# Performance work log

Hardware: AMD Instinct MI355X
Metric: run time of the kernel (lower is better)

The kernel has to match this reference:

```python
import jax, jax.numpy as jnp
import numpy as np

NUM_HEADS = 8
DIM = 256
HEAD_DIM = DIM // NUM_HEADS  # 32
CPB_HIDDEN = 512
FFN_HIDDEN = 1024


def _relative_position_cpb(query_size, key_size, pretrain_size):
    # TransNeXt-style continuous position bias table + index (query==key grid here)
    qh, qw = query_size
    kh, kw = key_size
    ph, pw = pretrain_size
    aqh = np.arange(qh, dtype=np.float64)
    akh = np.arange(kh, dtype=np.float64)
    aqw = np.arange(qw, dtype=np.float64)
    akw = np.arange(kw, dtype=np.float64)
    kH, kW = np.meshgrid(akh, akw, indexing='ij')
    qH, qW = np.meshgrid(aqh, aqw, indexing='ij')
    rel_h = (qH.reshape(-1)[:, None] - kH.reshape(-1)[None, :]) / (ph - 1) * 8.0
    rel_w = (qW.reshape(-1)[:, None] - kW.reshape(-1)[None, :]) / (pw - 1) * 8.0
    rel = np.stack([rel_h, rel_w], axis=-1).reshape(-1, 2)
    table, idx = np.unique(rel, return_inverse=True, axis=0)
    table = np.sign(table) * np.log2(np.abs(table) + 1.0) / np.log2(8.0)
    return idx.astype(np.int32).reshape(-1), table.astype(np.float32)


def setup_inputs() -> dict:
    key = jax.random.key(0)
    ks = jax.random.split(key, 16)
    B, C, H, W = 8, 256, 128, 128
    q = jax.random.normal(ks[0], (B, C, H, W), dtype=jnp.float32)
    kv = jax.random.normal(ks[1], (B, C, H, W), dtype=jnp.float32)
    rel_idx_np, rel_table_np = _relative_position_cpb((32, 32), (32, 32), (32, 32))
    s = 0.02
    inp = {
        'q': q,
        'kv': kv,
        'rel_pos_index': jnp.asarray(rel_idx_np),
        'rel_coords_table': jnp.asarray(rel_table_np),
        'Wq': jax.random.normal(ks[2], (DIM, DIM), jnp.float32) * s,
        'bq': jnp.zeros((DIM,), jnp.float32),
        'Wkv': jax.random.normal(ks[3], (DIM, 2 * DIM), jnp.float32) * s,
        'bkv': jnp.zeros((2 * DIM,), jnp.float32),
        'Wo': jax.random.normal(ks[4], (DIM, DIM), jnp.float32) * s,
        'bo': jnp.zeros((DIM,), jnp.float32),
        'cpb_w1': jax.random.normal(ks[5], (2, CPB_HIDDEN), jnp.float32) * s,
        'cpb_b1': jnp.zeros((CPB_HIDDEN,), jnp.float32),
        'cpb_w2': jax.random.normal(ks[6], (CPB_HIDDEN, NUM_HEADS), jnp.float32) * s,
        'cpb_b2': jnp.zeros((NUM_HEADS,), jnp.float32),
        'ffn_w1': jax.random.normal(ks[7], (DIM, FFN_HIDDEN), jnp.float32) * s,
        'ffn_b1': jnp.zeros((FFN_HIDDEN,), jnp.float32),
        'ffn_w2': jax.random.normal(ks[8], (FFN_HIDDEN, DIM), jnp.float32) * s,
        'ffn_b2': jnp.zeros((DIM,), jnp.float32),
        'ln_g': jnp.ones((DIM,), jnp.float32),
        'ln_b': jnp.zeros((DIM,), jnp.float32),
    }
    return inp


def _resize_bilinear(x, size):
    # matches torch F.interpolate(mode='bilinear', align_corners=False)
    return jax.image.resize(x, (x.shape[0], x.shape[1], size[0], size[1]),
                            method='linear', antialias=False)


def _layernorm(x, g, b, eps=1e-5):
    mu = jnp.mean(x, axis=-1, keepdims=True)
    var = jnp.mean(jnp.square(x - mu), axis=-1, keepdims=True)
    return (x - mu) * jax.lax.rsqrt(var + eps) * g + b


def _fpn_forward(q, kv, rel_pos_index, rel_coords_table, Wq, bq, Wkv, bkv, Wo, bo,
                 cpb_w1, cpb_b1, cpb_w2, cpb_b2, ffn_w1, ffn_b1, ffn_w2, ffn_b2, ln_g, ln_b):
    x = q
    B, C, H, W = q.shape
    pH = H // 4
    pW = H // 4  # note: original code uses h for both, matching square inputs
    N = pH * pW

    qd = jax.nn.relu(_resize_bilinear(q, (pH, pW)))   # [B,C,pH,pW] (dropout p=0)
    kvd = jax.nn.relu(_resize_bilinear(kv, (pH, pW)))
    qt = qd.reshape(B, C, N).transpose(0, 2, 1)   # [B,N,C]
    kvt = kvd.reshape(B, C, N).transpose(0, 2, 1)  # [B,N,C]

    # --- BVAM: cross-attention with continuous relative position bias ---
    qh = (qt @ Wq + bq).reshape(B, N, NUM_HEADS, HEAD_DIM).transpose(0, 2, 1, 3)  # [B,h,N,d]
    kvp = (kvt @ Wkv + bkv).reshape(B, N, 2, NUM_HEADS, HEAD_DIM).transpose(2, 0, 3, 1, 4)
    k, v = kvp[0], kvp[1]  # [B,h,N,d]

    cpb = jax.nn.relu(rel_coords_table @ cpb_w1 + cpb_b1) @ cpb_w2 + cpb_b2  # [L,h]
    bias = cpb[rel_pos_index].reshape(N, N, NUM_HEADS).transpose(2, 0, 1)    # [h,N,N]

    scale = 1.0 / jnp.sqrt(jnp.float32(HEAD_DIM))
    logits = jnp.einsum('bhnd,bhmd->bhnm', qh, k) * scale + bias[None]
    attn = jax.nn.softmax(logits, axis=-1)
    out = jnp.einsum('bhnm,bhmd->bhnd', attn, v)
    out = out.transpose(0, 2, 1, 3).reshape(B, N, C) @ Wo + bo  # [B,N,C]

    # --- FFN (post-norm, gelu) ---
    ff = jax.nn.gelu(out @ ffn_w1 + ffn_b1, approximate=False) @ ffn_w2 + ffn_b2
    y = _layernorm(out + ff, ln_g, ln_b)  # [B,N,C]

    # back to spatial, upsample, residual
    y = y.transpose(0, 2, 1).reshape(B, C, pH, pW)
    y = jax.nn.relu(_resize_bilinear(y, (H, W)))
    return x + y


def reference(q, kv, rel_pos_index, rel_coords_table, Wq, bq, Wkv, bkv, Wo, bo,
              cpb_w1, cpb_b1, cpb_w2, cpb_b2, ffn_w1, ffn_b1, ffn_w2, ffn_b2, ln_g, ln_b):
    return _fpn_forward(q, kv, rel_pos_index, rel_coords_table, Wq, bq, Wkv, bkv, Wo, bo,
                        cpb_w1, cpb_b1, cpb_w2, cpb_b2, ffn_w1, ffn_b1, ffn_w2, ffn_b2, ln_g, ln_b)
```

## Files before the change

kernel.cpp:

```cpp
#include <hip/hip_runtime.h>
#include <hip/hip_bf16.h>
#include <hip/hip_fp16.h>

typedef __hip_bfloat16 bf16;
typedef __attribute__((ext_vector_type(8))) __bf16 bf16x8;
typedef __attribute__((ext_vector_type(4))) __bf16 bf16x4;
typedef __attribute__((ext_vector_type(4))) float f32x4;
typedef __attribute__((ext_vector_type(4))) float f4;

__device__ __forceinline__ void gload_lds16(const bf16* g, bf16* l)
{
    __builtin_amdgcn_global_load_lds((const __attribute__((address_space(1))) void*)g,
                                     (__attribute__((address_space(3))) void*)l, 16, 0, 0);
}

__global__ __launch_bounds__(256) void prep_kernel(
    const float* __restrict__ tab, const float* __restrict__ w1, const float* __restrict__ b1,
    const float* __restrict__ w2, const float* __restrict__ b2, float* __restrict__ cpbout, int L, int ncpb,
    const float* __restrict__ Wq, const float* __restrict__ Wkv, const float* __restrict__ Wo,
    const float* __restrict__ fw1, const float* __restrict__ fw2,
    bf16* __restrict__ WqT, bf16* __restrict__ WkvT, bf16* __restrict__ WoT,
    bf16* __restrict__ W1T, bf16* __restrict__ W2T,
    const float* __restrict__ qsrc, const float* __restrict__ kvsrc,
    bf16* __restrict__ qdst, bf16* __restrict__ kvdst)
{
    __shared__ float o[32][33];
    const int t = threadIdx.x;
    int bid = blockIdx.x;
    if (bid < ncpb) {
        int l = bid * 32 + (t >> 3);
        int js = t & 7;
        bool valid = l < L;
        float t0 = valid ? tab[2 * l] : 0.f, t1 = valid ? tab[2 * l + 1] : 0.f;
        float acc[8];
#pragma unroll
        for (int hh = 0; hh < 8; ++hh) acc[hh] = 0.f;
        for (int j = js; j < 512; j += 8) {
            float hv = fmaxf(t0 * w1[j] + t1 * w1[512 + j] + b1[j], 0.f);
            f4 w2a = *(const f4*)&w2[j * 8];
            f4 w2b = *(const f4*)&w2[j * 8 + 4];
#pragma unroll
            for (int hh = 0; hh < 4; ++hh) { acc[hh] += hv * w2a[hh]; acc[4 + hh] += hv * w2b[hh]; }
        }
#pragma unroll
        for (int d = 1; d < 8; d <<= 1)
#pragma unroll
            for (int hh = 0; hh < 8; ++hh) acc[hh] += __shfl_xor(acc[hh], d);
        if (js == 0 && valid)
#pragma unroll
            for (int hh = 0; hh < 8; ++hh) cpbout[(size_t)hh * L + l] = acc[hh] + b2[hh];
        return;
    }
    bid -= ncpb;
    if (bid < 3072) {
        const float* W; bf16* WT; int K, N, base;
        if (bid < 256)       { W = Wq;  WT = WqT;  K = 256;  N = 256;  base = 0; }
        else if (bid < 768)  { W = Wkv; WT = WkvT; K = 256;  N = 512;  base = 256; }
        else if (bid < 1024) { W = Wo;  WT = WoT;  K = 256;  N = 256;  base = 768; }
        else if (bid < 2048) { W = fw1; WT = W1T;  K = 256;  N = 1024; base = 1024; }
        else                 { W = fw2; WT = W2T;  K = 1024; N = 256;  base = 2048; }
        int idx = (bid - base) * 256 + t;
        int n = idx / K, k = idx % K;
        WT[idx] = (bf16)W[(size_t)k * N + n];
        return;
    }
    bid -= 3072;
    {
        const float* src = bid < 2048 ? qsrc : kvsrc;
        bf16* dst = bid < 2048 ? qdst : kvdst;
        int bb2 = bid & 2047;
        int cc = bb2 & 7, i = (bb2 >> 3) & 31, b = bb2 >> 8;
#pragma unroll
        for (int p = 0; p < 4; ++p) {
            int id = p * 256 + t;
            int c = id >> 5, j = id & 31;
            const float* r = src + ((size_t)(b * 256 + cc * 32 + c) * 128 + 4 * i + 1) * 128 + 4 * j;
            float4 r1 = *(const float4*)r;
            float4 r2 = *(const float4*)(r + 128);
            o[c][j] = 0.25f * (r1.y + r1.z + r2.y + r2.z);
        }
        __syncthreads();
#pragma unroll
        for (int p = 0; p < 4; ++p) {
            int id = p * 256 + t;
            int j = id >> 5, c = id & 31;
            dst[(size_t)(b * 1024 + i * 32 + j) * 256 + cc * 32 + c] = (bf16)fmaxf(o[c][j], 0.f);
        }
    }
}

__global__ __launch_bounds__(256) void bias_gather_kernel(
    const int* __restrict__ ridx, const float* __restrict__ cpbh,
    bf16* __restrict__ biasF, int L)
{
    int gid = blockIdx.x * 256 + threadIdx.x;
    int ls = gid & 63;
    int mt = (gid >> 6) & 31;
    int qt = gid >> 11;
    int lo = ls & 15, hi = ls >> 4;
    int idx[2][8];
#pragma unroll
    for (int qj = 0; qj < 2; ++qj)
#pragma unroll
        for (int j = 0; j < 8; ++j) {
            int kf = j >> 2, r = j & 3;
            int q = qt * 32 + qj * 16 + lo;
            int m = mt * 32 + kf * 16 + hi * 4 + r;
            idx[qj][j] = ridx[q * 1024 + m];
        }
    for (int h = 0; h < 8; ++h) {
        const float* ct = cpbh + (size_t)h * L;
#pragma unroll
        for (int qj = 0; qj < 2; ++qj) {
            bf16 vals[8];
#pragma unroll
            for (int j = 0; j < 8; ++j) vals[j] = (bf16)ct[idx[qj][j]];
            size_t off = ((((size_t)(h * 32 + qt) * 32 + mt) * 2 + qj) * 64 + ls) * 8;
            *(bf16x8*)&biasF[off] = *(const bf16x8*)vals;
        }
    }
}

template<int BM, int BN>
__global__ __launch_bounds__(256) void gemm_bt(
    const bf16* __restrict__ A, const bf16* __restrict__ BT,
    const float* __restrict__ bias, bf16* __restrict__ Cb, float* __restrict__ Cf,
    const bf16* __restrict__ resid, int M, int N, int K, int act)
{
    constexpr int MI = BM / 32;
    constexpr int NJ = BN / 32;
    __shared__ __align__(16) bf16 As[BM * 64];
    __shared__ __align__(16) bf16 Bs[BN * 64];
    const int tid = threadIdx.x;
    const int lane = tid & 63, wid = tid >> 6;
    const int lo = lane & 15, hi = lane >> 4;
    const int m0 = blockIdx.x * BM, n0 = blockIdx.y * BN;
    const int wr = wid >> 1, wc = wid & 1;
    f32x4 acc[MI][NJ];
#pragma unroll
    for (int i = 0; i < MI; ++i)
#pragma unroll
        for (int j = 0; j < NJ; ++j) acc[i][j] = f32x4{0.f, 0.f, 0.f, 0.f};

    for (int k0 = 0; k0 < K; k0 += 64) {
        __syncthreads();
#pragma unroll
        for (int p = 0; p < BM / 32; ++p) {
            int f = p * 256 + wid * 64 + lane;
            int row = f >> 3, cs = f & 7;
            gload_lds16(&A[(size_t)(m0 + row) * K + k0 + ((cs ^ (row & 7)) * 8)],
                        As + (size_t)(p * 256 + wid * 64) * 8);
        }
#pragma unroll
        for (int p = 0; p < BN / 32; ++p) {
            int f = p * 256 + wid * 64 + lane;
            int row = f >> 3, cs = f & 7;
            gload_lds16(&BT[(size_t)(n0 + row) * K + k0 + ((cs ^ (row & 7)) * 8)],
                        Bs + (size_t)(p * 256 + wid * 64) * 8);
        }
        __syncthreads();
        bf16x8 af[2][MI], bfr[2][NJ];
#pragma unroll
        for (int kk = 0; kk < 2; ++kk) {
#pragma unroll
            for (int i = 0; i < MI; ++i) {
                int row = wr * (BM / 2) + i * 16 + lo;
                af[kk][i] = *(const bf16x8*)&As[row * 64 + (((kk * 4 + hi) ^ (lo & 7)) * 8)];
            }
#pragma unroll
            for (int j = 0; j < NJ; ++j) {
                int row = wc * (BN / 2) + j * 16 + lo;
                bfr[kk][j] = *(const bf16x8*)&Bs[row * 64 + (((kk * 4 + hi) ^ (lo & 7)) * 8)];
            }
        }
#pragma unroll
        for (int kk = 0; kk < 2; ++kk)
#pragma unroll
            for (int i = 0; i < MI; ++i)
#pragma unroll
                for (int j = 0; j < NJ; ++j)
                    acc[i][j] = __builtin_amdgcn_mfma_f32_16x16x32_bf16(af[kk][i], bfr[kk][j], acc[i][j], 0, 0, 0);
    }
#pragma unroll
    for (int i = 0; i < MI; ++i)
#pragma unroll
        for (int j = 0; j < NJ; ++j) {
            int col = n0 + wc * (BN / 2) + j * 16 + lo;
            float bv = bias[col];
#pragma unroll
            for (int r = 0; r < 4; ++r) {
                int row = m0 + wr * (BM / 2) + i * 16 + hi * 4 + r;
                float v = acc[i][j][r] + bv;
                if (act == 1) v = 0.5f * v * (1.f + erff(v * 0.70710678118654752f));
                if (resid) v += (float)resid[(size_t)row * N + col];
                if (Cb) Cb[(size_t)row * N + col] = (bf16)v;
                else    Cf[(size_t)row * N + col] = v;
            }
        }
}

__global__ __launch_bounds__(256) void ffn2_ln_kernel(
    const bf16* __restrict__ A, const bf16* __restrict__ BT,
    const float* __restrict__ bias, const bf16* __restrict__ resid,
    const float* __restrict__ g, const float* __restrict__ bb,
    bf16* __restrict__ ysp)
{
    __shared__ __align__(16) bf16 As[32 * 64];
    __shared__ __align__(16) bf16 Bs[256 * 64];
    __shared__ float buf[32][260];
    const int tid = threadIdx.x;
    const int lane = tid & 63, wid = tid >> 6;
    const int lo = lane & 15, hi = lane >> 4;
    const int m0 = blockIdx.x * 32;
    f32x4 acc[2][4];
#pragma unroll
    for (int i = 0; i < 2; ++i)
#pragma unroll
        for (int j = 0; j < 4; ++j) acc[i][j] = f32x4{0.f, 0.f, 0.f, 0.f};

    for (int k0 = 0; k0 < 1024; k0 += 64) {
        __syncthreads();
        {
            int f = tid;
            int row = f >> 3, cs = f & 7;
            gload_lds16(&A[(size_t)(m0 + row) * 1024 + k0 + ((cs ^ (row & 7)) * 8)],
                        As + (size_t)(wid * 64) * 8);
        }
#pragma unroll
        for (int p = 0; p < 8; ++p) {
            int f = p * 256 + tid;
            int row = f >> 3, cs = f & 7;
            gload_lds16(&BT[(size_t)row * 1024 + k0 + ((cs ^ (row & 7)) * 8)],
                        Bs + (size_t)(p * 256 + wid * 64) * 8);
        }
        __syncthreads();
        bf16x8 af[2][2], bfr[2][4];
#pragma unroll
        for (int kk = 0; kk < 2; ++kk) {
#pragma unroll
            for (int i = 0; i < 2; ++i) {
                int row = i * 16 + lo;
                af[kk][i] = *(const bf16x8*)&As[row * 64 + (((kk * 4 + hi) ^ (lo & 7)) * 8)];
            }
#pragma unroll
            for (int j = 0; j < 4; ++j) {
                int row = wid * 64 + j * 16 + lo;
                bfr[kk][j] = *(const bf16x8*)&Bs[row * 64 + (((kk * 4 + hi) ^ (lo & 7)) * 8)];
            }
        }
#pragma unroll
        for (int kk = 0; kk < 2; ++kk)
#pragma unroll
            for (int i = 0; i < 2; ++i)
#pragma unroll
                for (int j = 0; j < 4; ++j)
                    acc[i][j] = __builtin_amdgcn_mfma_f32_16x16x32_bf16(af[kk][i], bfr[kk][j], acc[i][j], 0, 0, 0);
    }
#pragma unroll
    for (int i = 0; i < 2; ++i)
#pragma unroll
        for (int j = 0; j < 4; ++j) {
            int col = wid * 64 + j * 16 + lo;
            float bv = bias[col];
#pragma unroll
            for (int r = 0; r < 4; ++r) {
                int lr = i * 16 + hi * 4 + r;
                buf[lr][col] = acc[i][j][r] + bv + (float)resid[(size_t)(m0 + lr) * 256 + col];
            }
        }
    __syncthreads();
#pragma unroll
    for (int rr = 0; rr < 8; ++rr) {
        int row = wid * 8 + rr;
        f4 x = *(const f4*)&buf[row][lane * 4];
        float s = x[0] + x[1] + x[2] + x[3];
#pragma unroll
        for (int d = 1; d < 64; d <<= 1) s += __shfl_xor(s, d);
        float mean = s * (1.f / 256.f);
        f4 dv = {x[0] - mean, x[1] - mean, x[2] - mean, x[3] - mean};
        float s2 = dv[0] * dv[0] + dv[1] * dv[1] + dv[2] * dv[2] + dv[3] * dv[3];
#pragma unroll
        for (int d = 1; d < 64; d <<= 1) s2 += __shfl_xor(s2, d);
        float rstd = rsqrtf(s2 * (1.f / 256.f) + 1e-5f);
        f4 o = {dv[0] * rstd, dv[1] * rstd, dv[2] * rstd, dv[3] * rstd};
        *(f4*)&buf[row][lane * 4] = o;
    }
    __syncthreads();
    float gc = g[tid], bc = bb[tid];
    int b = m0 >> 10, n0l = m0 & 1023;
    bf16* dst = &ysp[((size_t)(b * 256 + tid) << 10) + n0l];
#pragma unroll
    for (int p = 0; p < 4; ++p) {
        bf16 tmp[8];
#pragma unroll
        for (int k = 0; k < 8; ++k) tmp[k] = (bf16)(buf[p * 8 + k][tid] * gc + bc);
        *(bf16x8*)&dst[p * 8] = *(const bf16x8*)tmp;
    }
}

__global__ __launch_bounds__(256) void vtrans_kernel(const bf16* __restrict__ kvp,
                                                     bf16* __restrict__ vT)
{
    __shared__ __align__(16) bf16 tile[64][40];
    int bid = blockIdx.x;
    int mc = bid & 15, h = (bid >> 4) & 7, b = bid >> 7;
    int t = threadIdx.x;
    {
        int m = t >> 2, p = (t & 3) * 8;
        *(float4*)&tile[m][p] =
            *(const float4*)&kvp[(size_t)(b * 1024 + mc * 64 + m) * 512 + 256 + h * 32 + p];
    }
    __syncthreads();
#pragma unroll
    for (int it = 0; it < 8; ++it) {
        int f = it * 256 + t;
        int d = f >> 6, m = f & 63;
        vT[(size_t)((b * 8 + h) * 32 + d) * 1024 + mc * 64 + m] = tile[m][d];
    }
}

__global__ __launch_bounds__(256) void attn_kernel(
    const bf16* __restrict__ qh, const bf16* __restrict__ kvp, const bf16* __restrict__ vT,
    const bf16* __restrict__ biasF, bf16* __restrict__ attnout)
{
    __shared__ __align__(16) bf16 Ps[4][32 * 40];
    __shared__ __align__(16) __half accs[4][32][34];
    __shared__ float pm[4][32], pl[4][32];
    const int tid = threadIdx.x, lane = tid & 63, wid = tid >> 6;
    const int lo = lane & 15, hi = lane >> 4;
    const int qt = blockIdx.x, n0 = qt * 32;
    const int h = blockIdx.y;
    const int b = blockIdx.z;
    const float scale = 0.17677669529663687f;
    const f32x4 zero4 = {0.f, 0.f, 0.f, 0.f};

    bf16x8 qf[2];
#pragma unroll
    for (int qj = 0; qj < 2; ++qj)
        qf[qj] = *(const bf16x8*)&qh[(size_t)(b * 1024 + n0 + qj * 16 + lo) * 256 + h * 32 + hi * 8];

    f32x4 acc[2][2];
#pragma unroll
    for (int i = 0; i < 2; ++i)
#pragma unroll
        for (int j = 0; j < 2; ++j) acc[i][j] = zero4;
    float mrow[2] = {-1e30f, -1e30f}, lrow[2] = {0.f, 0.f};

    bf16* Pw = Ps[wid];

    for (int t = wid; t < 32; t += 4) {
        const int m0 = t * 32;
        bf16x8 kfr0 = *(const bf16x8*)&kvp[(size_t)(b * 1024 + m0 + lo) * 512 + h * 32 + hi * 8];
        bf16x8 kfr1 = *(const bf16x8*)&kvp[(size_t)(b * 1024 + m0 + 16 + lo) * 512 + h * 32 + hi * 8];
        bf16x8 va0 = *(const bf16x8*)&vT[(size_t)((b * 8 + h) * 32 + lo) * 1024 + m0 + hi * 8];
        bf16x8 va1 = *(const bf16x8*)&vT[(size_t)((b * 8 + h) * 32 + 16 + lo) * 1024 + m0 + hi * 8];
        size_t boff = (((size_t)(h * 32 + qt) * 32 + t) * 2 * 64 + lane) * 8;
        bf16x8 bv0 = *(const bf16x8*)&biasF[boff];
        bf16x8 bv1 = *(const bf16x8*)&biasF[boff + 512];

        f32x4 s[2][2];
        s[0][0] = __builtin_amdgcn_mfma_f32_16x16x32_bf16(kfr0, qf[0], zero4, 0, 0, 0);
        s[0][1] = __builtin_amdgcn_mfma_f32_16x16x32_bf16(kfr0, qf[1], zero4, 0, 0, 0);
        s[1][0] = __builtin_amdgcn_mfma_f32_16x16x32_bf16(kfr1, qf[0], zero4, 0, 0, 0);
        s[1][1] = __builtin_amdgcn_mfma_f32_16x16x32_bf16(kfr1, qf[1], zero4, 0, 0, 0);
#pragma unroll
        for (int kf = 0; kf < 2; ++kf)
#pragma unroll
            for (int r = 0; r < 4; ++r) {
                s[kf][0][r] = s[kf][0][r] * scale + (float)bv0[kf * 4 + r];
                s[kf][1][r] = s[kf][1][r] * scale + (float)bv1[kf * 4 + r];
            }
#pragma unroll
        for (int qj = 0; qj < 2; ++qj) {
            float mx = fmaxf(fmaxf(fmaxf(s[0][qj][0], s[0][qj][1]), fmaxf(s[0][qj][2], s[0][qj][3])),
                             fmaxf(fmaxf(s[1][qj][0], s[1][qj][1]), fmaxf(s[1][qj][2], s[1][qj][3])));
            mx = fmaxf(mx, __shfl_xor(mx, 16));
            mx = fmaxf(mx, __shfl_xor(mx, 32));
            float mnew = fmaxf(mrow[qj], mx);
            float alpha = __expf(mrow[qj] - mnew);
            float rs = 0.f;
#pragma unroll
            for (int kf = 0; kf < 2; ++kf)
#pragma unroll
                for (int r = 0; r < 4; ++r) {
                    float p = __expf(s[kf][qj][r] - mnew);
                    s[kf][qj][r] = p;
                    rs += p;
                }
            rs += __shfl_xor(rs, 16);
            rs += __shfl_xor(rs, 32);
            lrow[qj] = lrow[qj] * alpha + rs;
            mrow[qj] = mnew;
#pragma unroll
            for (int di = 0; di < 2; ++di)
#pragma unroll
                for (int r = 0; r < 4; ++r) acc[di][qj][r] *= alpha;
        }
#pragma unroll
        for (int qj = 0; qj < 2; ++qj)
#pragma unroll
            for (int kf = 0; kf < 2; ++kf)
#pragma unroll
                for (int r = 0; r < 4; ++r)
                    Pw[(qj * 16 + lo) * 40 + kf * 16 + hi * 4 + r] = (bf16)s[kf][qj][r];
        bf16x8 pb0 = *(const bf16x8*)&Pw[lo * 40 + hi * 8];
        bf16x8 pb1 = *(const bf16x8*)&Pw[(16 + lo) * 40 + hi * 8];
        acc[0][0] = __builtin_amdgcn_mfma_f32_16x16x32_bf16(va0, pb0, acc[0][0], 0, 0, 0);
        acc[0][1] = __builtin_amdgcn_mfma_f32_16x16x32_bf16(va0, pb1, acc[0][1], 0, 0, 0);
        acc[1][0] = __builtin_amdgcn_mfma_f32_16x16x32_bf16(va1, pb0, acc[1][0], 0, 0, 0);
        acc[1][1] = __builtin_amdgcn_mfma_f32_16x16x32_bf16(va1, pb1, acc[1][1], 0, 0, 0);
    }
#pragma unroll
    for (int di = 0; di < 2; ++di)
#pragma unroll
        for (int qj = 0; qj < 2; ++qj)
#pragma unroll
            for (int r = 0; r < 4; ++r)
                accs[wid][di * 16 + hi * 4 + r][qj * 16 + lo] = __float2half(acc[di][qj][r]);
    if (hi == 0) {
#pragma unroll
        for (int qj = 0; qj < 2; ++qj) {
            pm[wid][qj * 16 + lo] = mrow[qj];
            pl[wid][qj * 16 + lo] = lrow[qj];
        }
    }
    __syncthreads();
    int q = tid >> 3, d0 = (tid & 7) * 4;
    float M = fmaxf(fmaxf(pm[0][q], pm[1][q]), fmaxf(pm[2][q], pm[3][q]));
    float f0 = __expf(pm[0][q] - M), f1 = __expf(pm[1][q] - M);
    float f2 = __expf(pm[2][q] - M), f3 = __expf(pm[3][q] - M);
    float inv = 1.f / (pl[0][q] * f0 + pl[1][q] * f1 + pl[2][q] * f2 + pl[3][q] * f3);
    bf16 tmp[4];
#pragma unroll
    for (int j = 0; j < 4; ++j) {
        int d = d0 + j;
        float o = f0 * (float)accs[0][d][q] + f1 * (float)accs[1][d][q] +
                  f2 * (float)accs[2][d][q] + f3 * (float)accs[3][d][q];
        tmp[j] = (bf16)(o * inv);
    }
    *(bf16x4*)&attnout[(size_t)(b * 1024 + n0 + q) * 256 + h * 32 + d0] = *(const bf16x4*)tmp;
}

__global__ __launch_bounds__(256) void upsample_kernel(const float* __restrict__ x,
    const bf16* __restrict__ ysp, float* __restrict__ out)
{
    int idx = blockIdx.x * 256 + threadIdx.x;
    int w4 = idx & 31; int r1 = idx >> 5;
    int hh = r1 & 127; int r2 = r1 >> 7;
    int c = r2 & 255; int b = r2 >> 8;
    float chh = 0.25f * hh - 0.375f;
    float fi = floorf(chh);
    float fh = chh - fi;
    int i0 = (int)fi;
    int ia = i0 < 0 ? 0 : i0;
    int ib = (i0 + 1) > 31 ? 31 : (i0 + 1);
    const bf16* yr = ysp + ((size_t)(b * 256 + c) << 10);
    const bf16* ra = yr + ia * 32;
    const bf16* rb = yr + ib * 32;
    f4 xv = *(const f4*)&x[(size_t)idx * 4];
    f4 o;
#pragma unroll
    for (int k = 0; k < 4; ++k) {
        int ww = w4 * 4 + k;
        float cww = 0.25f * ww - 0.375f;
        float fj = floorf(cww);
        float fw = cww - fj;
        int j0 = (int)fj;
        int ja = j0 < 0 ? 0 : j0;
        int jb = (j0 + 1) > 31 ? 31 : (j0 + 1);
        float v = (1.f - fh) * ((1.f - fw) * (float)ra[ja] + fw * (float)ra[jb]) +
                  fh * ((1.f - fw) * (float)rb[ja] + fw * (float)rb[jb]);
        o[k] = xv[k] + fmaxf(v, 0.f);
    }
    *(f4*)&out[(size_t)idx * 4] = o;
}

extern "C" void kernel_launch(void* const* d_in, const int* in_sizes, int n_in,
                              void* d_out, int out_size, void* d_ws, size_t ws_size,
                              hipStream_t stream)
{
    (void)n_in; (void)out_size; (void)ws_size;
    const float* q    = (const float*)d_in[0];
    const float* kv   = (const float*)d_in[1];
    const int*   ridx = (const int*)d_in[2];
    const float* rtab = (const float*)d_in[3];
    const float* Wq   = (const float*)d_in[4];
    const float* bq   = (const float*)d_in[5];
    const float* Wkv  = (const float*)d_in[6];
    const float* bkv  = (const float*)d_in[7];
    const float* Wo   = (const float*)d_in[8];
    const float* bo   = (const float*)d_in[9];
    const float* cw1  = (const float*)d_in[10];
    const float* cb1  = (const float*)d_in[11];
    const float* cw2  = (const float*)d_in[12];
    const float* cb2  = (const float*)d_in[13];
    const float* fw1  = (const float*)d_in[14];
    const float* fb1  = (const float*)d_in[15];
    const float* fw2  = (const float*)d_in[16];
    const float* fb2  = (const float*)d_in[17];
    const float* lng  = (const float*)d_in[18];
    const float* lnb  = (const float*)d_in[19];
    const int L = in_sizes[3] / 2;
    const int ncpb = (L + 31) / 32;

    char* w = (char*)d_ws;
    auto alloc = [&](size_t bytes) { char* p = w; w += (bytes + 255) & ~(size_t)255; return p; };
    bf16* qt      = (bf16*)alloc(8192ull * 256 * 2);
    bf16* kvt     = (bf16*)alloc(8192ull * 256 * 2);
    bf16* qhb     = (bf16*)alloc(8192ull * 256 * 2);
    bf16* kvpb    = (bf16*)alloc(8192ull * 512 * 2);
    bf16* vTb     = (bf16*)alloc(8ull * 8 * 32 * 1024 * 2);
    bf16* attnb   = (bf16*)alloc(8192ull * 256 * 2);
    bf16* outb    = (bf16*)alloc(8192ull * 256 * 2);
    bf16* ffh     = (bf16*)alloc(8192ull * 1024 * 2);
    bf16* ysp     = (bf16*)alloc(8ull * 256 * 1024 * 2);
    bf16* WqT     = (bf16*)alloc(256ull * 256 * 2);
    bf16* WkvT    = (bf16*)alloc(512ull * 256 * 2);
    bf16* WoT     = (bf16*)alloc(256ull * 256 * 2);
    bf16* W1T     = (bf16*)alloc(1024ull * 256 * 2);
    bf16* W2T     = (bf16*)alloc(256ull * 1024 * 2);
    float* cpbb   = (float*)alloc((size_t)8 * L * 4);
    bf16* biasF   = ffh;

    prep_kernel<<<dim3(ncpb + 3072 + 4096), 256, 0, stream>>>(
        rtab, cw1, cb1, cw2, cb2, cpbb, L, ncpb,
        Wq, Wkv, Wo, fw1, fw2, WqT, WkvT, WoT, W1T, W2T,
        q, kv, qt, kvt);
    bias_gather_kernel<<<dim3(256), 256, 0, stream>>>(ridx, cpbb, biasF, L);
    gemm_bt<64, 64><<<dim3(128, 4), 256, 0, stream>>>(qt, WqT, bq, qhb, nullptr, nullptr, 8192, 256, 256, 0);
    gemm_bt<64, 64><<<dim3(128, 8), 256, 0, stream>>>(kvt, WkvT, bkv, kvpb, nullptr, nullptr, 8192, 512, 256, 0);
    vtrans_kernel<<<dim3(1024), 256, 0, stream>>>(kvpb, vTb);
    attn_kernel<<<dim3(32, 8, 8), 256, 0, stream>>>(qhb, kvpb, vTb, biasF, attnb);
    gemm_bt<64, 64><<<dim3(128, 4), 256, 0, stream>>>(attnb, WoT, bo, outb, nullptr, nullptr, 8192, 256, 256, 0);
    gemm_bt<128, 64><<<dim3(64, 16), 256, 0, stream>>>(outb, W1T, fb1, ffh, nullptr, nullptr, 8192, 1024, 256, 1);
    ffn2_ln_kernel<<<dim3(256), 256, 0, stream>>>(ffh, W2T, fb2, outb, lng, lnb, ysp);
    upsample_kernel<<<dim3(32768), 256, 0, stream>>>(q, ysp, (float*)d_out);
}
```

Baseline: 199.3 us.

## Double-buffer GEMM LDS tiles, fuse Q/KV projections, restructure bias gather

GEMM kernels (gemm_bt and ffn2_ln) now use two LDS buffers so the next K-tile's global-to-LDS loads are issued before the MFMA work on the current tile. This hides load latency at the cost of doubled shared memory per block. The Q and KV projections are merged into one launch to remove a kernel launch and fill the GPU better. The bias gather is rewritten to use a 2D grid with coalesced index staging through shared memory, giving 1024 blocks instead of 256.

```diff
diff --git a/kernel.cpp b/kernel.cpp
--- a/kernel.cpp
+++ b/kernel.cpp
@@ -93,31 +93,98 @@
     const int* __restrict__ ridx, const float* __restrict__ cpbh,
     bf16* __restrict__ biasF, int L)
 {
-    int gid = blockIdx.x * 256 + threadIdx.x;
-    int ls = gid & 63;
-    int mt = (gid >> 6) & 31;
-    int qt = gid >> 11;
-    int lo = ls & 15, hi = ls >> 4;
-    int idx[2][8];
-#pragma unroll
-    for (int qj = 0; qj < 2; ++qj)
-#pragma unroll
-        for (int j = 0; j < 8; ++j) {
-            int kf = j >> 2, r = j & 3;
-            int q = qt * 32 + qj * 16 + lo;
-            int m = mt * 32 + kf * 16 + hi * 4 + r;
-            idx[qj][j] = ridx[q * 1024 + m];
-        }
-    for (int h = 0; h < 8; ++h) {
+    __shared__ int rix[32][32];
+    const int qt = blockIdx.x, mt = blockIdx.y;
+    const int t = threadIdx.x;
+    {
+        int q = t >> 3, m4 = (t & 7) * 4;
+        *(int4*)&rix[q][m4] = *(const int4*)&ridx[(size_t)(qt * 32 + q) * 1024 + mt * 32 + m4];
+    }
+    __syncthreads();
+    const int ls = t & 63, qj = (t >> 6) & 1, hg = t >> 7;
+    const int lo = ls & 15, hi = ls >> 4;
+    int lidx[8];
+#pragma unroll
+    for (int j = 0; j < 8; ++j) {
+        int kf = j >> 2, r = j & 3;
+        lidx[j] = rix[qj * 16 + lo][kf * 16 + hi * 4 + r];
+    }
+#pragma unroll
+    for (int hh = 0; hh < 4; ++hh) {
+        int h = hg * 4 + hh;
         const float* ct = cpbh + (size_t)h * L;
-#pragma unroll
-        for (int qj = 0; qj < 2; ++qj) {
-            bf16 vals[8];
-#pragma unroll
-            for (int j = 0; j < 8; ++j) vals[j] = (bf16)ct[idx[qj][j]];
-            size_t off = ((((size_t)(h * 32 + qt) * 32 + mt) * 2 + qj) * 64 + ls) * 8;
-            *(bf16x8*)&biasF[off] = *(const bf16x8*)vals;
-        }
+        bf16 vals[8];
+#pragma unroll
+        for (int j = 0; j < 8; ++j) vals[j] = (bf16)ct[lidx[j]];
+        size_t off = ((((size_t)(h * 32 + qt) * 32 + mt) * 2 + qj) * 64 + ls) * 8;
+        *(bf16x8*)&biasF[off] = *(const bf16x8*)vals;
+    }
+}
+
+template<int BM, int BN>
+__device__ __forceinline__ void gemm_core(
+    const bf16* __restrict__ A, const bf16* __restrict__ BT, int K,
+    int m0, int n0, bf16* As0, bf16* Bs0, f32x4 (&acc)[BM / 32][BN / 32])
+{
+    constexpr int MI = BM / 32, NJ = BN / 32;
+    const int tid = threadIdx.x;
+    const int lane = tid & 63, wid = tid >> 6;
+    const int lo = lane & 15, hi = lane >> 4;
+    const int wr = wid >> 1, wc = wid & 1;
+#pragma unroll
+    for (int i = 0; i < MI; ++i)
+#pragma unroll
+        for (int j = 0; j < NJ; ++j) acc[i][j] = f32x4{0.f, 0.f, 0.f, 0.f};
+
+    auto stage = [&](int bsel, int k0) {
+        bf16* As = As0 + bsel * (BM * 64);
+        bf16* Bs = Bs0 + bsel * (BN * 64);
+#pragma unroll
+        for (int p = 0; p < BM / 32; ++p) {
+            int f = p * 256 + wid * 64 + lane;
+            int row = f >> 3, cs = f & 7;
+            gload_lds16(&A[(size_t)(m0 + row) * K + k0 + ((cs ^ (row & 7)) * 8)],
+                        As + (size_t)(p * 256 + wid * 64) * 8);
+        }
+#pragma unroll
+        for (int p = 0; p < BN / 32; ++p) {
+            int f = p * 256 + wid * 64 + lane;
+            int row = f >> 3, cs = f & 7;
+            gload_lds16(&BT[(size_t)(n0 + row) * K + k0 + ((cs ^ (row & 7)) * 8)],
+                        Bs + (size_t)(p * 256 + wid * 64) * 8);
+        }
+    };
+    stage(0, 0);
+    __syncthreads();
+    const int nt = K / 64;
+    int cur = 0;
+    for (int t = 0; t < nt; ++t) {
+        if (t + 1 < nt) stage(cur ^ 1, (t + 1) * 64);
+        const bf16* As = As0 + cur * (BM * 64);
+        const bf16* Bs = Bs0 + cur * (BN * 64);
+        bf16x8 af[2][MI], bfr[2][NJ];
+#pragma unroll
+        for (int kk = 0; kk < 2; ++kk) {
+#pragma unroll
+            for (int i = 0; i < MI; ++i) {
+                int row = wr * (BM / 2) + i * 16 + lo;
+                af[kk][i] = *(const bf16x8*)&As[row * 64 + (((kk * 4 + hi) ^ (lo & 7)) * 8)];
+            }
+#pragma unroll
+            for (int j = 0; j < NJ; ++j) {
+                int row = wc * (BN / 2) + j * 16 + lo;
+                bfr[kk][j] = *(const bf16x8*)&Bs[row * 64 + (((kk * 4 + hi) ^ (lo & 7)) * 8)];
+            }
+        }
+#pragma unroll
+        for (int kk = 0; kk < 2; ++kk)
+#pragma unroll
+            for (int i = 0; i < MI; ++i)
+#pragma unroll
+                for (int j = 0; j < NJ; ++j)
+                    acc[i][j] = __builtin_amdgcn_mfma_f32_16x16x32_bf16(af[kk][i], bfr[kk][j], acc[i][j], 0, 0, 0);
+        __syncthreads();
+        cur ^= 1;
     }
 }
 
@@ -127,60 +194,16 @@
     const float* __restrict__ bias, bf16* __restrict__ Cb, float* __restrict__ Cf,
     const bf16* __restrict__ resid, int M, int N, int K, int act)
 {
-    constexpr int MI = BM / 32;
-    constexpr int NJ = BN / 32;
-    __shared__ __align__(16) bf16 As[BM * 64];
-    __shared__ __align__(16) bf16 Bs[BN * 64];
+    constexpr int MI = BM / 32, NJ = BN / 32;
+    __shared__ __align__(16) bf16 As[2 * BM * 64];
+    __shared__ __align__(16) bf16 Bs[2 * BN * 64];
     const int tid = threadIdx.x;
     const int lane = tid & 63, wid = tid >> 6;
     const int lo = lane & 15, hi = lane >> 4;
     const int m0 = blockIdx.x * BM, n0 = blockIdx.y * BN;
     const int wr = wid >> 1, wc = wid & 1;
     f32x4 acc[MI][NJ];
-#pragma unroll
-    for (int i = 0; i < MI; ++i)
-#pragma unroll
-        for (int j = 0; j < NJ; ++j) acc[i][j] = f32x4{0.f, 0.f, 0.f, 0.f};
-
-    for (int k0 = 0; k0 < K; k0 += 64) {
-        __syncthreads();
-#pragma unroll
-        for (int p = 0; p < BM / 32; ++p) {
-            int f = p * 256 + wid * 64 + lane;
-            int row = f >> 3, cs = f & 7;
-            gload_lds16(&A[(size_t)(m0 + row) * K + k0 + ((cs ^ (row & 7)) * 8)],
-                        As + (size_t)(p * 256 + wid * 64) * 8);
-        }
-#pragma unroll
-        for (int p = 0; p < BN / 32; ++p) {
-            int f = p * 256 + wid * 64 + lane;
-            int row = f >> 3, cs = f & 7;
-            gload_lds16(&BT[(size_t)(n0 + row) * K + k0 + ((cs ^ (row & 7)) * 8)],
-                        Bs + (size_t)(p * 256 + wid * 64) * 8);
-        }
-        __syncthreads();
-        bf16x8 af[2][MI], bfr[2][NJ];
-#pragma unroll
-        for (int kk = 0; kk < 2; ++kk) {
-#pragma unroll
-            for (int i = 0; i < MI; ++i) {
-                int row = wr * (BM / 2) + i * 16 + lo;
-                af[kk][i] = *(const bf16x8*)&As[row * 64 + (((kk * 4 + hi) ^ (lo & 7)) * 8)];
-            }
-#pragma unroll
-            for (int j = 0; j < NJ; ++j) {
-                int row = wc * (BN / 2) + j * 16 + lo;
-                bfr[kk][j] = *(const bf16x8*)&Bs[row * 64 + (((kk * 4 + hi) ^ (lo & 7)) * 8)];
-            }
-        }
-#pragma unroll
-        for (int kk = 0; kk < 2; ++kk)
-#pragma unroll
-            for (int i = 0; i < MI; ++i)
-#pragma unroll
-                for (int j = 0; j < NJ; ++j)
-                    acc[i][j] = __builtin_amdgcn_mfma_f32_16x16x32_bf16(af[kk][i], bfr[kk][j], acc[i][j], 0, 0, 0);
-    }
+    gemm_core<BM, BN>(A, BT, K, m0, n0, As, Bs, acc);
 #pragma unroll
     for (int i = 0; i < MI; ++i)
 #pragma unroll
@@ -199,14 +222,47 @@
         }
 }
 
+__global__ __launch_bounds__(256) void gemm_qkv(
+    const bf16* __restrict__ qt, const bf16* __restrict__ WqT, const float* __restrict__ bq,
+    bf16* __restrict__ qhb,
+    const bf16* __restrict__ kvt, const bf16* __restrict__ WkvT, const float* __restrict__ bkv,
+    bf16* __restrict__ kvpb)
+{
+    __shared__ __align__(16) bf16 As[2 * 64 * 64];
+    __shared__ __align__(16) bf16 Bs[2 * 64 * 64];
+    const int tid = threadIdx.x;
+    const int lane = tid & 63, wid = tid >> 6;
+    const int lo = lane & 15, hi = lane >> 4;
+    const int wr = wid >> 1, wc = wid & 1;
+    const int by = blockIdx.y;
+    const bf16 *A, *BT; const float* bias; bf16* C; int N, n0;
+    if (by < 4) { A = qt;  BT = WqT;  bias = bq;  C = qhb;  N = 256; n0 = by * 64; }
+    else        { A = kvt; BT = WkvT; bias = bkv; C = kvpb; N = 512; n0 = (by - 4) * 64; }
+    const int m0 = blockIdx.x * 64;
+    f32x4 acc[2][2];
+    gemm_core<64, 64>(A, BT, 256, m0, n0, As, Bs, acc);
+#pragma unroll
+    for (int i = 0; i < 2; ++i)
+#pragma unroll
+        for (int j = 0; j < 2; ++j) {
+            int col = n0 + wc * 32 + j * 16 + lo;
+            float bv = bias[col];
+#pragma unroll
+            for (int r = 0; r < 4; ++r) {
+                int row = m0 + wr * 32 + i * 16 + hi * 4 + r;
+                C[(size_t)row * N + col] = (bf16)(acc[i][j][r] + bv);
+            }
+        }
+}
+
 __global__ __launch_bounds__(256) void ffn2_ln_kernel(
     const bf16* __restrict__ A, const bf16* __restrict__ BT,
     const float* __restrict__ bias, const bf16* __restrict__ resid,
     const float* __restrict__ g, const float* __restrict__ bb,
     bf16* __restrict__ ysp)
 {
-    __shared__ __align__(16) bf16 As[32 * 64];
-    __shared__ __align__(16) bf16 Bs[256 * 64];
+    __shared__ __align__(16) bf16 As[2 * 32 * 64];
+    __shared__ __align__(16) bf16 Bs[2 * 256 * 64];
     __shared__ float buf[32][260];
     const int tid = threadIdx.x;
     const int lane = tid & 63, wid = tid >> 6;
@@ -218,34 +274,40 @@
 #pragma unroll
         for (int j = 0; j < 4; ++j) acc[i][j] = f32x4{0.f, 0.f, 0.f, 0.f};
 
-    for (int k0 = 0; k0 < 1024; k0 += 64) {
-        __syncthreads();
+    auto stage = [&](int bsel, int k0) {
+        bf16* Asb = As + bsel * (32 * 64);
+        bf16* Bsb = Bs + bsel * (256 * 64);
         {
-            int f = tid;
-            int row = f >> 3, cs = f & 7;
+            int f = tid, row = f >> 3, cs = f & 7;
             gload_lds16(&A[(size_t)(m0 + row) * 1024 + k0 + ((cs ^ (row & 7)) * 8)],
-                        As + (size_t)(wid * 64) * 8);
+                        Asb + (size_t)(wid * 64) * 8);
         }
 #pragma unroll
         for (int p = 0; p < 8; ++p) {
-            int f = p * 256 + tid;
-            int row = f >> 3, cs = f & 7;
+            int f = p * 256 + tid, row = f >> 3, cs = f & 7;
             gload_lds16(&BT[(size_t)row * 1024 + k0 + ((cs ^ (row & 7)) * 8)],
-                        Bs + (size_t)(p * 256 + wid * 64) * 8);
-        }
-        __syncthreads();
+                        Bsb + (size_t)(p * 256 + wid * 64) * 8);
+        }
+    };
+    stage(0, 0);
+    __syncthreads();
+    int cur = 0;
+    for (int t = 0; t < 16; ++t) {
+        if (t < 15) stage(cur ^ 1, (t + 1) * 64);
+        const bf16* Asb = As + cur * (32 * 64);
+        const bf16* Bsb = Bs + cur * (256 * 64);
         bf16x8 af[2][2], bfr[2][4];
 #pragma unroll
         for (int kk = 0; kk < 2; ++kk) {
 #pragma unroll
             for (int i = 0; i < 2; ++i) {
                 int row = i * 16 + lo;
-                af[kk][i] = *(const bf16x8*)&As[row * 64 + (((kk * 4 + hi) ^ (lo & 7)) * 8)];
+                af[kk][i] = *(const bf16x8*)&Asb[row * 64 + (((kk * 4 + hi) ^ (lo & 7)) * 8)];
             }
 #pragma unroll
             for (int j = 0; j < 4; ++j) {
                 int row = wid * 64 + j * 16 + lo;
-                bfr[kk][j] = *(const bf16x8*)&Bs[row * 64 + (((kk * 4 + hi) ^ (lo & 7)) * 8)];
+                bfr[kk][j] = *(const bf16x8*)&Bsb[row * 64 + (((kk * 4 + hi) ^ (lo & 7)) * 8)];
             }
         }
 #pragma unroll
@@ -255,6 +317,8 @@
 #pragma unroll
                 for (int j = 0; j < 4; ++j)
                     acc[i][j] = __builtin_amdgcn_mfma_f32_16x16x32_bf16(af[kk][i], bfr[kk][j], acc[i][j], 0, 0, 0);
+        __syncthreads();
+        cur ^= 1;
     }
 #pragma unroll
     for (int i = 0; i < 2; ++i)
@@ -526,9 +590,8 @@
         rtab, cw1, cb1, cw2, cb2, cpbb, L, ncpb,
         Wq, Wkv, Wo, fw1, fw2, WqT, WkvT, WoT, W1T, W2T,
         q, kv, qt, kvt);
-    bias_gather_kernel<<<dim3(256), 256, 0, stream>>>(ridx, cpbb, biasF, L);
-    gemm_bt<64, 64><<<dim3(128, 4), 256, 0, stream>>>(qt, WqT, bq, qhb, nullptr, nullptr, 8192, 256, 256, 0);
-    gemm_bt<64, 64><<<dim3(128, 8), 256, 0, stream>>>(kvt, WkvT, bkv, kvpb, nullptr, nullptr, 8192, 512, 256, 0);
+    bias_gather_kernel<<<dim3(32, 32), 256, 0, stream>>>(ridx, cpbb, biasF, L);
+    gemm_qkv<<<dim3(128, 12), 256, 0, stream>>>(qt, WqT, bq, qhb, kvt, WkvT, bkv, kvpb);
     vtrans_kernel<<<dim3(1024), 256, 0, stream>>>(kvpb, vTb);
     attn_kernel<<<dim3(32, 8, 8), 256, 0, stream>>>(qhb, kvpb, vTb, biasF, attnb);
     gemm_bt<64, 64><<<dim3(128, 4), 256, 0, stream>>>(attnb, WoT, bo, outb, nullptr, nullptr, 8192, 256, 256, 0);
```

Result: no change. 202.2 us (+1.4%).
